# Kernel tuning notes

Hardware: AMD Instinct MI355X
Metric: run time of the kernel (lower is better)

## Reference

```python
import jax, jax.numpy as jnp
import numpy as np

D_MODEL = 1024
NUM_HEADS = 16
D_FF = 4096
MAX_SEQ_LEN = 2048
THETA = 10000.0
EPS = 1e-5
B, S = 2, 2048


def setup_inputs() -> dict:
    key = jax.random.key(0)
    ks = jax.random.split(key, 10)
    scale = 0.02
    inp = {
        "in_features": jax.random.normal(ks[0], (B, S, D_MODEL), dtype=jnp.float32),
        "token_positions": jnp.broadcast_to(jnp.arange(S, dtype=jnp.int32), (B, S)),
        "q_w": jax.random.normal(ks[1], (D_MODEL, D_MODEL), dtype=jnp.float32) * scale,
        "k_w": jax.random.normal(ks[2], (D_MODEL, D_MODEL), dtype=jnp.float32) * scale,
        "v_w": jax.random.normal(ks[3], (D_MODEL, D_MODEL), dtype=jnp.float32) * scale,
        "o_w": jax.random.normal(ks[4], (D_MODEL, D_MODEL), dtype=jnp.float32) * scale,
        "ln1_w": jnp.ones((D_MODEL,), dtype=jnp.float32),
        "ln2_w": jnp.ones((D_MODEL,), dtype=jnp.float32),
        "ffn_w1": jax.random.normal(ks[5], (D_FF, D_MODEL), dtype=jnp.float32) * scale,
        "ffn_w2": jax.random.normal(ks[6], (D_MODEL, D_FF), dtype=jnp.float32) * scale,
        "ffn_w3": jax.random.normal(ks[7], (D_FF, D_MODEL), dtype=jnp.float32) * scale,
    }
    return inp


def _rmsnorm(x, w, eps=EPS):
    return x * jax.lax.rsqrt(jnp.mean(x * x, axis=-1, keepdims=True) + eps) * w


def _rope(x, pos, theta=THETA):
    # x: [B, H, S, Dh]; pos: [B, S] int
    dh = x.shape[-1]
    inv_freq = theta ** (-jnp.arange(0, dh, 2, dtype=jnp.float32) / dh)  # [Dh/2]
    ang = pos.astype(jnp.float32)[..., None] * inv_freq                  # [B, S, Dh/2]
    cos = jnp.cos(ang)[:, None, :, :]  # [B, 1, S, Dh/2]
    sin = jnp.sin(ang)[:, None, :, :]
    x1, x2 = x[..., 0::2], x[..., 1::2]
    r1 = x1 * cos - x2 * sin
    r2 = x1 * sin + x2 * cos
    return jnp.stack([r1, r2], axis=-1).reshape(x.shape)


def _block(x, pos, q_w, k_w, v_w, o_w, ln1_w, ln2_w, w1, w2, w3):
    b, s, d = x.shape
    h, dh = NUM_HEADS, d // NUM_HEADS
    # Pre-LN attention
    xn = _rmsnorm(x, ln1_w)
    q = jnp.einsum('bsd,ed->bse', xn, q_w).reshape(b, s, h, dh).transpose(0, 2, 1, 3)
    k = jnp.einsum('bsd,ed->bse', xn, k_w).reshape(b, s, h, dh).transpose(0, 2, 1, 3)
    v = jnp.einsum('bsd,ed->bse', xn, v_w).reshape(b, s, h, dh).transpose(0, 2, 1, 3)
    q = _rope(q, pos)
    k = _rope(k, pos)
    scores = jnp.einsum('bhqd,bhkd->bhqk', q, k) / jnp.sqrt(jnp.float32(dh))
    causal = jnp.tril(jnp.ones((s, s), dtype=bool))
    scores = jnp.where(causal, scores, jnp.float32(-1e9))
    attn = jax.nn.softmax(scores, axis=-1)
    ctx = jnp.einsum('bhqk,bhkd->bhqd', attn, v).transpose(0, 2, 1, 3).reshape(b, s, d)
    attn_out = jnp.einsum('bsd,ed->bse', ctx, o_w)
    x = x + attn_out
    # Pre-LN SwiGLU FFN
    xn2 = _rmsnorm(x, ln2_w)
    g = jnp.einsum('bsd,fd->bsf', xn2, w1)
    u = jnp.einsum('bsd,fd->bsf', xn2, w3)
    ffn_out = jnp.einsum('bsf,df->bsd', jax.nn.silu(g) * u, w2)
    return x + ffn_out


def reference(in_features, token_positions, q_w, k_w, v_w, o_w, ln1_w, ln2_w, ffn_w1, ffn_w2, ffn_w3):
    return _block(in_features, token_positions, q_w, k_w, v_w, o_w, ln1_w, ln2_w, ffn_w1, ffn_w2, ffn_w3)
```

## Files before the change

kernel.cpp:

```cpp
#include <hip/hip_runtime.h>
#include <hip/hip_bf16.h>

typedef __attribute__((ext_vector_type(8))) __bf16 bf16x8;
typedef __attribute__((ext_vector_type(4))) float f32x4;
typedef __attribute__((ext_vector_type(16))) float f32x16;

#define DEV static __device__ __forceinline__

DEV unsigned short f2bf(float f) {
  __bf16 h = (__bf16)f;
  union { __bf16 h; unsigned short u; } v; v.h = h;
  return v.u;
}
DEV float bf2f(unsigned short h) {
  union { unsigned int u; float f; } v; v.u = ((unsigned int)h) << 16;
  return v.f;
}
DEV unsigned pkbf(float lo, float hi) {
  union { __bf16 h[2]; unsigned u; } v;
  v.h[0] = (__bf16)lo; v.h[1] = (__bf16)hi;
  return v.u;
}
DEV f32x4 mfma16(bf16x8 a, bf16x8 b, f32x4 c) {
  return __builtin_amdgcn_mfma_f32_16x16x32_bf16(a, b, c, 0, 0, 0);
}
DEV f32x16 mfma32(bf16x8 a, bf16x8 b, f32x16 c) {
  return __builtin_amdgcn_mfma_f32_32x32x16_bf16(a, b, c, 0, 0, 0);
}
DEV void gload_lds16(const void* g, void* l) {
  __builtin_amdgcn_global_load_lds((__attribute__((address_space(1))) void*)g,
                                   (__attribute__((address_space(3))) void*)l,
                                   16, 0, 0);
}
DEV float fexp2(float x) { return exp2f(x); }

struct CvtArgs { const float* src[7]; int cum[8]; };
__global__ __launch_bounds__(256) void cvt_all(CvtArgs a, unsigned short* __restrict__ dst) {
  int i = (blockIdx.x * 256 + threadIdx.x) * 4;
  if (i >= a.cum[7]) return;
  int w = 0;
#pragma unroll 7
  for (int t = 0; t < 7; ++t) if (i >= a.cum[t + 1]) w = t + 1;
  float4 v = *(const float4*)(a.src[w] + (i - a.cum[w]));
  dst[i + 0] = f2bf(v.x);
  dst[i + 1] = f2bf(v.y);
  dst[i + 2] = f2bf(v.z);
  dst[i + 3] = f2bf(v.w);
}

__global__ __launch_bounds__(256) void rmsnorm_k(const float* __restrict__ x,
                                                 const float* __restrict__ w,
                                                 unsigned short* __restrict__ out) {
  int row = blockIdx.x;
  int tid = threadIdx.x;
  const float* xr = x + (size_t)row * 1024;
  float4 v = *(const float4*)(xr + tid * 4);
  float ss = v.x * v.x + v.y * v.y + v.z * v.z + v.w * v.w;
#pragma unroll
  for (int m = 32; m >= 1; m >>= 1) ss += __shfl_xor(ss, m);
  __shared__ float red[4];
  int wid = tid >> 6;
  if ((tid & 63) == 0) red[wid] = ss;
  __syncthreads();
  float tot = red[0] + red[1] + red[2] + red[3];
  float rs = rsqrtf(tot * (1.0f / 1024.0f) + 1e-5f);
  float4 wv = *(const float4*)(w + tid * 4);
  unsigned short* o = out + (size_t)row * 1024 + tid * 4;
  o[0] = f2bf(v.x * rs * wv.x);
  o[1] = f2bf(v.y * rs * wv.y);
  o[2] = f2bf(v.z * rs * wv.z);
  o[3] = f2bf(v.w * rs * wv.w);
}

__global__ __launch_bounds__(256) void rope2_k(unsigned short* __restrict__ q,
                                               unsigned short* __restrict__ k,
                                               const int* __restrict__ pos) {
  int gid = blockIdx.x * 256 + threadIdx.x;
  unsigned short* x = (gid < 2097152) ? q : k;
  int idx = gid & 2097151;
  int i = idx & 31;
  int s = (idx >> 5) & 2047;
  int bh = idx >> 16;
  int b = bh >> 4;
  float p = (float)pos[b * 2048 + s];
  float inv = exp2f(-(float)i * 0.4152410118609203f);
  float ang = p * inv;
  float sn = sinf(ang), cs = cosf(ang);
  size_t base = (((size_t)bh * 2048) + s) * 64 + 2 * i;
  float x1 = bf2f(x[base]), x2 = bf2f(x[base + 1]);
  x[base]     = f2bf(x1 * cs - x2 * sn);
  x[base + 1] = f2bf(x1 * sn + x2 * cs);
}

template <int MODE>
DEV void gemm8_body(const unsigned short* __restrict__ A, int lda,
                    const unsigned short* __restrict__ B, int ldb,
                    int bm, int bn, int kbase, int nt,
                    unsigned short* __restrict__ outb, float* __restrict__ outf,
                    const float* __restrict__ resid, const unsigned short* __restrict__ gate,
                    unsigned short* As, unsigned short* Bs) {
  const int tid = threadIdx.x;
  const int lane = tid & 63, wid = tid >> 6;
  const int wr = wid >> 2, wc = wid & 3;
  const int m0 = bm * 256, n0 = bn * 256;

  const int r0 = tid >> 2, r1 = 128 + (tid >> 2), cc = tid & 3;
  const int sc0 = (cc ^ ((r0 >> 1) & 3)) * 8;
  const int sc1 = (cc ^ ((r1 >> 1) & 3)) * 8;
  const size_t arow0 = (size_t)(m0 + r0) * lda, arow1 = (size_t)(m0 + r1) * lda;
  const size_t brow0 = (size_t)(n0 + r0) * ldb, brow1 = (size_t)(n0 + r1) * ldb;
  const int du0 = tid * 8, du1 = (512 + tid) * 8;

  auto stA = [&](int t, int kh) {
    unsigned short* d = As + ((((t & 1) << 1) | kh) * 8192);
    const unsigned short* s = A + kbase + t * 64 + kh * 32;
    gload_lds16(s + arow0 + sc0, d + du0);
    gload_lds16(s + arow1 + sc1, d + du1);
  };
  auto stB = [&](int t, int kh) {
    unsigned short* d = Bs + ((((t & 1) << 1) | kh) * 8192);
    const unsigned short* s = B + kbase + t * 64 + kh * 32;
    gload_lds16(s + brow0 + sc0, d + du0);
    gload_lds16(s + brow1 + sc1, d + du1);
  };

  const int fcol = ((lane >> 4) ^ ((lane >> 1) & 3)) * 8;
  const int frow = lane & 15;
  const int abase = (wr * 128 + frow) * 32 + fcol;
  const int bbase = (wc * 64 + frow) * 32 + fcol;

  f32x4 acc[8][4] = {};
  bf16x8 a[4], b[4];

#define LOADA(buf, ks, mh) { const unsigned short* p_ = As + (((buf) << 1) | (ks)) * 8192 + abase + (mh) * 2048; \
  a[0] = *(const bf16x8*)(p_); a[1] = *(const bf16x8*)(p_ + 512); \
  a[2] = *(const bf16x8*)(p_ + 1024); a[3] = *(const bf16x8*)(p_ + 1536); }
#define LOADB(buf, ks) { const unsigned short* p_ = Bs + (((buf) << 1) | (ks)) * 8192 + bbase; \
  b[0] = *(const bf16x8*)(p_); b[1] = *(const bf16x8*)(p_ + 512); \
  b[2] = *(const bf16x8*)(p_ + 1024); b[3] = *(const bf16x8*)(p_ + 1536); }
#define MFMAQ(mh) { _Pragma("unroll") for (int fi = 0; fi < 4; ++fi) \
  _Pragma("unroll") for (int j = 0; j < 4; ++j) \
    acc[(mh) * 4 + fi][j] = mfma16(a[fi], b[j], acc[(mh) * 4 + fi][j]); }
#define LGK0() { asm volatile("s_waitcnt lgkmcnt(0)" ::: "memory"); __builtin_amdgcn_sched_barrier(0); }

  stA(0, 0); stB(0, 0); stA(0, 1); stB(0, 1);
  stA(1, 0); stB(1, 0);
  asm volatile("s_waitcnt vmcnt(4)" ::: "memory");
  __builtin_amdgcn_s_barrier();

  for (int t = 0; t < nt; ++t) {
    const int buf = t & 1;
    LOADA(buf, 0, 0); LOADB(buf, 0);
    if (t + 1 < nt) stA(t + 1, 1);
    __builtin_amdgcn_s_barrier();
    LGK0();
    __builtin_amdgcn_s_setprio(1); MFMAQ(0); __builtin_amdgcn_s_setprio(0);
    __builtin_amdgcn_s_barrier();
    LOADA(buf, 0, 1);
    if (t + 1 < nt) stB(t + 1, 1);
    __builtin_amdgcn_s_barrier();
    LGK0();
    __builtin_amdgcn_s_setprio(1); MFMAQ(1); __builtin_amdgcn_s_setprio(0);
    __builtin_amdgcn_s_barrier();
    LOADA(buf, 1, 0); LOADB(buf, 1);
    if (t + 2 < nt) stA(t + 2, 0);
    __builtin_amdgcn_s_barrier();
    LGK0();
    __builtin_amdgcn_s_setprio(1); MFMAQ(0); __builtin_amdgcn_s_setprio(0);
    __builtin_amdgcn_s_barrier();
    LOADA(buf, 1, 1);
    if (t + 2 < nt) stB(t + 2, 0);
    __builtin_amdgcn_s_barrier();
    LGK0();
    __builtin_amdgcn_s_setprio(1); MFMAQ(1); __builtin_amdgcn_s_setprio(0);
    if (t + 1 < nt) {
      if (t + 2 < nt) { asm volatile("s_waitcnt vmcnt(4)" ::: "memory"); }
      else            { asm volatile("s_waitcnt vmcnt(0)" ::: "memory"); }
      __builtin_amdgcn_s_barrier();
    }
  }
#undef LOADA
#undef LOADB
#undef MFMAQ
#undef LGK0

#pragma unroll
  for (int i = 0; i < 8; ++i)
#pragma unroll
    for (int j = 0; j < 4; ++j)
#pragma unroll
      for (int r = 0; r < 4; ++r) {
        int m = m0 + wr * 128 + i * 16 + ((lane >> 4) << 2) + r;
        int n = n0 + wc * 64 + j * 16 + (lane & 15);
        float v = acc[i][j][r];
        if (MODE == 0) {
          unsigned short* dst = outb + ((n >= 1024) ? 4194304 : 0);
          int nn = n & 1023;
          int bb = m >> 11, s = m & 2047, hh = nn >> 6, dd = nn & 63;
          dst[(((size_t)bb * 16 + hh) * 2048 + s) * 64 + dd] = f2bf(v);
        } else if (MODE == 1) {
          int hh = m >> 6, dd = m & 63, bb = n >> 11, s = n & 2047;
          outb[(((size_t)bb * 16 + hh) * 64 + dd) * 2048 + s] = f2bf(v);
        } else if (MODE == 2) {
          size_t idx = (size_t)m * 1024 + n;
          outf[idx] = resid[idx] + v;
        } else if (MODE == 3) {
          outb[(size_t)m * 4096 + n] = f2bf(v);
        } else if (MODE == 4) {
          size_t idx = (size_t)m * 4096 + n;
          float g = bf2f(gate[idx]);
          outb[idx] = f2bf(g / (1.0f + __expf(-g)) * v);
        } else {
          outf[(size_t)m * 1024 + n] = v;
        }
      }
}

DEV void swz_map(int bid, int nwg, int MT, int& bm, int& bn) {
  int cpx = nwg >> 3;
  int sw = (bid & 7) * cpx + (bid >> 3);
  bm = sw % MT;
  bn = sw / MT;
}

template <int MODE>
__global__ __launch_bounds__(512, 2) void gemm8_k(const unsigned short* __restrict__ A, int lda,
                                                  const unsigned short* __restrict__ B, int ldb,
                                                  int MT, int kz, int nt,
                                                  unsigned short* __restrict__ outb,
                                                  float* __restrict__ outf,
                                                  const float* __restrict__ resid,
                                                  const unsigned short* __restrict__ gate) {
  __shared__ __align__(16) unsigned short lds[65536];
  int bm, bn;
  swz_map(blockIdx.x, gridDim.x, MT, bm, bn);
  int kb = kz * blockIdx.y;
  float* of = outf;
  if (MODE == 5) of += (size_t)blockIdx.y * 4194304;
  gemm8_body<MODE>(A, lda, B, ldb, bm, bn, kb, nt, outb, of, resid, gate, lds, lds + 32768);
}

__global__ __launch_bounds__(512, 2) void gemm8_qkv(const unsigned short* __restrict__ xn,
                                                    const unsigned short* __restrict__ wqk,
                                                    const unsigned short* __restrict__ wv,
                                                    unsigned short* __restrict__ qk_out,
                                                    unsigned short* __restrict__ vt_out) {
  __shared__ __align__(16) unsigned short lds[65536];
  int bid = blockIdx.x;
  if (bid < 128) {
    int bm, bn;
    swz_map(bid, 128, 16, bm, bn);
    gemm8_body<0>(xn, 1024, wqk, 1024, bm, bn, 0, 16, qk_out, nullptr, nullptr, nullptr, lds, lds + 32768);
  } else {
    bid -= 128;
    int bm, bn;
    swz_map(bid, 64, 4, bm, bn);
    gemm8_body<1>(wv, 1024, xn, 1024, bm, bn, 0, 16, vt_out, nullptr, nullptr, nullptr, lds, lds + 32768);
  }
}

__global__ __launch_bounds__(256) void gemm_wo(const unsigned short* __restrict__ A,
                                               const unsigned short* __restrict__ Bw,
                                               float* __restrict__ outf,
                                               const float* __restrict__ resid) {
  __shared__ __align__(16) unsigned short As[128 * 64];
  __shared__ __align__(16) unsigned short Bs[128 * 64];
  const int K = 1024, N = 1024;
  const int tid = threadIdx.x;
  const int wid = tid >> 6, lane = tid & 63;
  const int wr = wid >> 1, wc = wid & 1;
  const int m0 = blockIdx.x * 128, n0 = blockIdx.y * 128;
  const int sw = (lane & 7) * 8;
  f32x4 acc[4][4] = {};

  for (int k0 = 0; k0 < K; k0 += 64) {
    __syncthreads();
#pragma unroll
    for (int it = 0; it < 4; ++it) {
      int c = wid * 4 + it;
      int row = c * 8 + (lane >> 3);
      int col = ((lane & 7) ^ (row & 7)) * 8;
      gload_lds16(A + (size_t)(m0 + row) * K + k0 + col, As + c * 512);
      gload_lds16(Bw + (size_t)(n0 + row) * K + k0 + col, Bs + c * 512);
    }
    asm volatile("s_waitcnt vmcnt(0)" ::: "memory");
    __syncthreads();
#pragma unroll
    for (int kk = 0; kk < 2; ++kk) {
      const int kof = (kk * 32 + (lane >> 4) * 8) ^ sw;
      bf16x8 af[4], bfr[4];
#pragma unroll
      for (int i = 0; i < 4; ++i) {
        af[i]  = *(const bf16x8*)(As + (wr * 64 + i * 16 + (lane & 15)) * 64 + kof);
        bfr[i] = *(const bf16x8*)(Bs + (wc * 64 + i * 16 + (lane & 15)) * 64 + kof);
      }
#pragma unroll
      for (int i = 0; i < 4; ++i)
#pragma unroll
        for (int j = 0; j < 4; ++j) acc[i][j] = mfma16(af[i], bfr[j], acc[i][j]);
    }
  }
  const int rb = m0 + wr * 64 + ((lane >> 4) * 4);
  const int cb = n0 + wc * 64 + (lane & 15);
#pragma unroll
  for (int i = 0; i < 4; ++i)
#pragma unroll
    for (int r = 0; r < 4; ++r) {
      int m = rb + i * 16 + r;
#pragma unroll
      for (int j = 0; j < 4; ++j) {
        size_t idx = (size_t)m * N + cb + j * 16;
        outf[idx] = resid[idx] + acc[i][j][r];
      }
    }
}

__global__ __launch_bounds__(256) void reduce_k(float* __restrict__ out,
                                                const float* __restrict__ part) {
  int i = (blockIdx.x * 256 + threadIdx.x) * 4;
  float4 o = *(const float4*)(out + i);
  float4 p0 = *(const float4*)(part + i);
  float4 p1 = *(const float4*)(part + 4194304 + i);
  float4 p2 = *(const float4*)(part + 8388608 + i);
  float4 p3 = *(const float4*)(part + 12582912 + i);
  o.x += p0.x + p1.x + p2.x + p3.x;
  o.y += p0.y + p1.y + p2.y + p3.y;
  o.z += p0.z + p1.z + p2.z + p3.z;
  o.w += p0.w + p1.w + p2.w + p3.w;
  *(float4*)(out + i) = o;
}

__global__ __launch_bounds__(256) void attn_k(const unsigned short* __restrict__ q,
                                              const unsigned short* __restrict__ k,
                                              const unsigned short* __restrict__ vt,
                                              unsigned short* __restrict__ ctx) {
  __shared__ __align__(16) unsigned short Ks[2][4096];
  __shared__ __align__(16) unsigned short Vs[2][4096];
  const int bid = blockIdx.x;
  const int bh = (bid & 7) * 4 + ((bid >> 3) & 3);
  const int qtile = 15 - (bid >> 5);
  const int tid = threadIdx.x, wid = tid >> 6, lane = tid & 63;
  const int l31 = lane & 31, hi = lane >> 5;
  const size_t bhS = (size_t)bh * 2048;
  const size_t bhD = (size_t)bh * 64 * 2048;
  const int b = bh >> 4, hh = bh & 15;
  const float SC2 = 0.18033688011112042f;

  const int c0 = wid * 2, c1 = c0 + 1;
  const int rl0 = c0 * 4 + (lane >> 4), rl1 = c1 * 4 + (lane >> 4);
  const int u0 = ((lane & 15) ^ (rl0 & 15)) * 8;
  const int u1 = ((lane & 15) ^ (rl1 & 15)) * 8;
  const int sr0 = rl0 + ((u0 >> 6) << 5), scol0 = u0 & 63;
  const int sr1 = rl1 + ((u1 >> 6) << 5), scol1 = u1 & 63;

  auto stage = [&](int kt, int buf) {
    gload_lds16(k + (bhS + kt * 64 + sr0) * 64 + scol0, &Ks[buf][c0 * 512]);
    gload_lds16(k + (bhS + kt * 64 + sr1) * 64 + scol1, &Ks[buf][c1 * 512]);
    gload_lds16(vt + bhD + (size_t)sr0 * 2048 + kt * 64 + scol0, &Vs[buf][c0 * 512]);
    gload_lds16(vt + bhD + (size_t)sr1 * 2048 + kt * 64 + scol1, &Vs[buf][c1 * 512]);
  };

  const int qrow = qtile * 128 + wid * 32 + l31;
  bf16x8 qf[4];
  {
    const unsigned short* qp = q + (bhS + qrow) * 64 + hi * 8;
#pragma unroll
    for (int c = 0; c < 4; ++c) {
      bf16x8 t = *(const bf16x8*)(qp + c * 16);
#pragma unroll
      for (int j = 0; j < 8; ++j) t[j] = (__bf16)((float)t[j] * SC2);
      qf[c] = t;
    }
  }

  float mrow = -1e30f, lrow = 0.0f;
  f32x16 o0 = {}, o1 = {};
  const int qw0 = qtile * 128 + wid * 32;
  const int ktmax = (qw0 + 31) >> 6;
  const int KT = 2 * qtile + 2;
  const int rsw = (l31 & 15) * 8;

  stage(0, 0);
  stage(1, 1);
  asm volatile("s_waitcnt vmcnt(4)" ::: "memory");
  __builtin_amdgcn_s_barrier();

  for (int kt = 0; kt < KT; ++kt) {
    const int cur = kt & 1;
    if (kt <= ktmax) {
      f32x16 sa0 = {}, sa1 = {};
#pragma unroll
      for (int c = 0; c < 4; ++c) {
        int colbase = c * 16 + hi * 8;
        bf16x8 k0 = *(const bf16x8*)(&Ks[cur][l31 * 128 + (colbase ^ rsw)]);
        bf16x8 k1 = *(const bf16x8*)(&Ks[cur][l31 * 128 + ((64 + colbase) ^ rsw)]);
        sa0 = mfma32(k0, qf[c], sa0);
        sa1 = mfma32(k1, qf[c], sa1);
      }
      float s[32];
#pragma unroll
      for (int r = 0; r < 16; ++r) { s[r] = sa0[r]; s[16 + r] = sa1[r]; }
      if (kt * 64 + 63 > qw0) {
        const int qg = qw0 + l31;
#pragma unroll
        for (int r = 0; r < 16; ++r) {
          int key0 = kt * 64 + (r & 3) + 8 * (r >> 2) + 4 * hi;
          if (key0 > qg) s[r] = -3e38f;
          if (key0 + 32 > qg) s[16 + r] = -3e38f;
        }
      }
      float pmax = s[0];
#pragma unroll
      for (int r = 1; r < 32; ++r) pmax = fmaxf(pmax, s[r]);
      pmax = fmaxf(pmax, __shfl_xor(pmax, 32));
      if (!__all(pmax <= mrow + 11.5f)) {
        float mnew = fmaxf(mrow, pmax);
        float dl = mrow - mnew;
        mrow = mnew;
        lrow *= fexp2(dl);
#pragma unroll
        for (int r = 0; r < 16; ++r) {
          int qsrc = (r & 3) + 8 * (r >> 2) + 4 * hi;
          float ar = fexp2(__shfl(dl, qsrc, 64));
          o0[r] *= ar; o1[r] *= ar;
        }
      }
      float sum = 0.0f;
#pragma unroll
      for (int r = 0; r < 32; ++r) { s[r] = fexp2(s[r] - mrow); sum += s[r]; }
      lrow += sum;
      unsigned pw[16];
#pragma unroll
      for (int i = 0; i < 16; ++i) pw[i] = pkbf(s[2 * i], s[2 * i + 1]);
#pragma unroll
      for (int g = 0; g < 4; ++g) {
        asm volatile("v_permlane32_swap_b32 %0, %1" : "+v"(pw[4 * g]), "+v"(pw[4 * g + 2]));
        asm volatile("v_permlane32_swap_b32 %0, %1" : "+v"(pw[4 * g + 1]), "+v"(pw[4 * g + 3]));
      }
#pragma unroll
      for (int g = 0; g < 4; ++g) {
        union { unsigned w[4]; bf16x8 v; } pa;
        pa.w[0] = pw[4 * g]; pa.w[1] = pw[4 * g + 1];
        pa.w[2] = pw[4 * g + 2]; pa.w[3] = pw[4 * g + 3];
        int kl = g * 16 + hi * 8;
        bf16x8 v0 = *(const bf16x8*)(&Vs[cur][l31 * 128 + (kl ^ rsw)]);
        bf16x8 v1 = *(const bf16x8*)(&Vs[cur][l31 * 128 + ((64 + kl) ^ rsw)]);
        o0 = mfma32(pa.v, v0, o0);
        o1 = mfma32(pa.v, v1, o1);
      }
    }
    __builtin_amdgcn_s_barrier();
    if (kt + 2 < KT) {
      stage(kt + 2, cur);
      asm volatile("s_waitcnt vmcnt(4)" ::: "memory");
    } else if (kt + 1 < KT) {
      asm volatile("s_waitcnt vmcnt(0)" ::: "memory");
    }
    __builtin_amdgcn_s_barrier();
  }

  lrow += __shfl_xor(lrow, 32);
  float inv = 1.0f / lrow;
#pragma unroll
  for (int r = 0; r < 16; ++r) {
    int qsrc = (r & 3) + 8 * (r >> 2) + 4 * hi;
    float li = __shfl(inv, qsrc, 64);
    int srow = qtile * 128 + wid * 32 + qsrc;
    size_t base = ((size_t)b * 2048 + srow) * 1024 + hh * 64 + l31;
    ctx[base]      = f2bf(o0[r] * li);
    ctx[base + 32] = f2bf(o1[r] * li);
  }
}

extern "C" void kernel_launch(void* const* d_in, const int* in_sizes, int n_in,
                              void* d_out, int out_size, void* d_ws, size_t ws_size,
                              hipStream_t stream) {
  (void)in_sizes; (void)n_in; (void)out_size; (void)ws_size;
  const float* in_f = (const float*)d_in[0];
  const int* pos    = (const int*)d_in[1];
  const float* q_w  = (const float*)d_in[2];
  const float* k_w  = (const float*)d_in[3];
  const float* v_w  = (const float*)d_in[4];
  const float* o_w  = (const float*)d_in[5];
  const float* ln1  = (const float*)d_in[6];
  const float* ln2  = (const float*)d_in[7];
  const float* w1   = (const float*)d_in[8];
  const float* w2   = (const float*)d_in[9];
  const float* w3   = (const float*)d_in[10];
  float* out = (float*)d_out;

  unsigned short* ws = (unsigned short*)d_ws;
  unsigned short* wb   = ws;
  unsigned short* wqkb = wb;
  unsigned short* wvb  = wb + 2097152;
  unsigned short* wob  = wb + 3145728;
  unsigned short* w1b  = wb + 4194304;
  unsigned short* w2b  = wb + 8388608;
  unsigned short* w3b  = wb + 12582912;
  unsigned short* xn   = ws + 16777216;
  unsigned short* qb   = ws + 20971520;
  unsigned short* kb   = ws + 25165824;
  unsigned short* vb   = ws + 29360128;
  unsigned short* cx   = ws + 33554432;
  unsigned short* gb   = ws + 37748736;
  float* part          = (float*)(ws + 20971520);
  unsigned short* hb   = ws + 54525952;

  CvtArgs ca;
  ca.src[0] = q_w; ca.src[1] = k_w; ca.src[2] = v_w; ca.src[3] = o_w;
  ca.src[4] = w1;  ca.src[5] = w2;  ca.src[6] = w3;
  ca.cum[0] = 0;        ca.cum[1] = 1048576;  ca.cum[2] = 2097152;  ca.cum[3] = 3145728;
  ca.cum[4] = 4194304;  ca.cum[5] = 8388608;  ca.cum[6] = 12582912; ca.cum[7] = 16777216;
  cvt_all<<<16384, 256, 0, stream>>>(ca, wb);

  rmsnorm_k<<<4096, 256, 0, stream>>>(in_f, ln1, xn);

  gemm8_qkv<<<192, 512, 0, stream>>>(xn, wqkb, wvb, qb, vb);

  rope2_k<<<16384, 256, 0, stream>>>(qb, kb, pos);

  attn_k<<<512, 256, 0, stream>>>(qb, kb, vb, cx);

  gemm_wo<<<dim3(32, 8), 256, 0, stream>>>(cx, wob, out, in_f);

  rmsnorm_k<<<4096, 256, 0, stream>>>(out, ln2, xn);

  gemm8_k<3><<<256, 512, 0, stream>>>(xn, 1024, w1b, 1024, 16, 0, 16, gb, nullptr, nullptr, nullptr);
  gemm8_k<4><<<256, 512, 0, stream>>>(xn, 1024, w3b, 1024, 16, 0, 16, hb, nullptr, nullptr, gb);
  gemm8_k<5><<<dim3(64, 4), 512, 0, stream>>>(hb, 4096, w2b, 4096, 16, 1024, 16, nullptr, part, nullptr, nullptr);

  reduce_k<<<4096, 256, 0, stream>>>(out, part);
}
```

Before: 302.0 us.

## Split attention KV range across two wave groups with in-block softmax merge

Doubles the attention block to 512 threads. The two 4-wave groups each process half of the causal key tiles for the same 128 query rows, with their own double-buffered LDS staging. At the end, group 1 writes its partial output (as bf16) and its running max and sum to LDS, and group 0 merges them flash-decoding style before writing ctx. The aim is to halve the serial key-loop length per block and raise parallelism on long-causal tiles. In exchange it uses more LDS and registers per block, adds a merge step, and rounds the partial output to bf16 before merging.

Measured after the change: 314.0 us. 4.0% more time.

```diff
diff --git a/kernel.cpp b/kernel.cpp
--- a/kernel.cpp
+++ b/kernel.cpp
@@ -330,37 +330,45 @@
   *(float4*)(out + i) = o;
 }
 
-__global__ __launch_bounds__(256) void attn_k(const unsigned short* __restrict__ q,
-                                              const unsigned short* __restrict__ k,
-                                              const unsigned short* __restrict__ vt,
-                                              unsigned short* __restrict__ ctx) {
-  __shared__ __align__(16) unsigned short Ks[2][4096];
-  __shared__ __align__(16) unsigned short Vs[2][4096];
+__global__ __launch_bounds__(512, 4) void attn_k(const unsigned short* __restrict__ q,
+                                                 const unsigned short* __restrict__ k,
+                                                 const unsigned short* __restrict__ vt,
+                                                 unsigned short* __restrict__ ctx) {
+  __shared__ __align__(16) unsigned short Ks[16384];
+  __shared__ __align__(16) unsigned short Vs[16384];
   const int bid = blockIdx.x;
-  const int bh = (bid & 7) * 4 + ((bid >> 3) & 3);
-  const int qtile = 15 - (bid >> 5);
+  const int xcd = bid & 7, inner = bid >> 3;
+  const int bh = xcd * 4 + (inner & 3);
+  const int qtile = 15 - (inner >> 2);
   const int tid = threadIdx.x, wid = tid >> 6, lane = tid & 63;
+  const int w4 = wid & 3, g = wid >> 2;
   const int l31 = lane & 31, hi = lane >> 5;
   const size_t bhS = (size_t)bh * 2048;
   const size_t bhD = (size_t)bh * 64 * 2048;
   const int b = bh >> 4, hh = bh & 15;
   const float SC2 = 0.18033688011112042f;
 
-  const int c0 = wid * 2, c1 = c0 + 1;
+  const int NT = qtile + 1;
+  const int kb = g * NT;
+
+  const int c0 = w4 * 2, c1 = c0 + 1;
   const int rl0 = c0 * 4 + (lane >> 4), rl1 = c1 * 4 + (lane >> 4);
   const int u0 = ((lane & 15) ^ (rl0 & 15)) * 8;
   const int u1 = ((lane & 15) ^ (rl1 & 15)) * 8;
   const int sr0 = rl0 + ((u0 >> 6) << 5), scol0 = u0 & 63;
   const int sr1 = rl1 + ((u1 >> 6) << 5), scol1 = u1 & 63;
-
-  auto stage = [&](int kt, int buf) {
-    gload_lds16(k + (bhS + kt * 64 + sr0) * 64 + scol0, &Ks[buf][c0 * 512]);
-    gload_lds16(k + (bhS + kt * 64 + sr1) * 64 + scol1, &Ks[buf][c1 * 512]);
-    gload_lds16(vt + bhD + (size_t)sr0 * 2048 + kt * 64 + scol0, &Vs[buf][c0 * 512]);
-    gload_lds16(vt + bhD + (size_t)sr1 * 2048 + kt * 64 + scol1, &Vs[buf][c1 * 512]);
+  unsigned short* KsG = Ks + g * 8192;
+  unsigned short* VsG = Vs + g * 8192;
+
+  auto stage = [&](int ktl, int buf) {
+    int kt = kb + ktl;
+    gload_lds16(k + (bhS + kt * 64 + sr0) * 64 + scol0, KsG + buf * 4096 + c0 * 512);
+    gload_lds16(k + (bhS + kt * 64 + sr1) * 64 + scol1, KsG + buf * 4096 + c1 * 512);
+    gload_lds16(vt + bhD + (size_t)sr0 * 2048 + kt * 64 + scol0, VsG + buf * 4096 + c0 * 512);
+    gload_lds16(vt + bhD + (size_t)sr1 * 2048 + kt * 64 + scol1, VsG + buf * 4096 + c1 * 512);
   };
 
-  const int qrow = qtile * 128 + wid * 32 + l31;
+  const int qrow = qtile * 128 + w4 * 32 + l31;
   bf16x8 qf[4];
   {
     const unsigned short* qp = q + (bhS + qrow) * 64 + hi * 8;
@@ -375,9 +383,7 @@
 
   float mrow = -1e30f, lrow = 0.0f;
   f32x16 o0 = {}, o1 = {};
-  const int qw0 = qtile * 128 + wid * 32;
-  const int ktmax = (qw0 + 31) >> 6;
-  const int KT = 2 * qtile + 2;
+  const int qw0 = qtile * 128 + w4 * 32;
   const int rsw = (l31 & 15) * 8;
 
   stage(0, 0);
@@ -385,90 +391,134 @@
   asm volatile("s_waitcnt vmcnt(4)" ::: "memory");
   __builtin_amdgcn_s_barrier();
 
-  for (int kt = 0; kt < KT; ++kt) {
-    const int cur = kt & 1;
-    if (kt <= ktmax) {
-      f32x16 sa0 = {}, sa1 = {};
-#pragma unroll
-      for (int c = 0; c < 4; ++c) {
-        int colbase = c * 16 + hi * 8;
-        bf16x8 k0 = *(const bf16x8*)(&Ks[cur][l31 * 128 + (colbase ^ rsw)]);
-        bf16x8 k1 = *(const bf16x8*)(&Ks[cur][l31 * 128 + ((64 + colbase) ^ rsw)]);
-        sa0 = mfma32(k0, qf[c], sa0);
-        sa1 = mfma32(k1, qf[c], sa1);
+  for (int ktl = 0; ktl < NT; ++ktl) {
+    const int cur = ktl & 1;
+    const int kt = kb + ktl;
+    f32x16 sa0 = {}, sa1 = {};
+#pragma unroll
+    for (int c = 0; c < 4; ++c) {
+      int colbase = c * 16 + hi * 8;
+      bf16x8 k0 = *(const bf16x8*)(&KsG[cur * 4096 + l31 * 128 + (colbase ^ rsw)]);
+      bf16x8 k1 = *(const bf16x8*)(&KsG[cur * 4096 + l31 * 128 + ((64 + colbase) ^ rsw)]);
+      sa0 = mfma32(k0, qf[c], sa0);
+      sa1 = mfma32(k1, qf[c], sa1);
+    }
+    float s[32];
+#pragma unroll
+    for (int r = 0; r < 16; ++r) { s[r] = sa0[r]; s[16 + r] = sa1[r]; }
+    if (kt * 64 + 63 > qw0) {
+      const int qg = qw0 + l31;
+#pragma unroll
+      for (int r = 0; r < 16; ++r) {
+        int key0 = kt * 64 + (r & 3) + 8 * (r >> 2) + 4 * hi;
+        if (key0 > qg) s[r] = -3e38f;
+        if (key0 + 32 > qg) s[16 + r] = -3e38f;
       }
-      float s[32];
-#pragma unroll
-      for (int r = 0; r < 16; ++r) { s[r] = sa0[r]; s[16 + r] = sa1[r]; }
-      if (kt * 64 + 63 > qw0) {
-        const int qg = qw0 + l31;
-#pragma unroll
-        for (int r = 0; r < 16; ++r) {
-          int key0 = kt * 64 + (r & 3) + 8 * (r >> 2) + 4 * hi;
-          if (key0 > qg) s[r] = -3e38f;
-          if (key0 + 32 > qg) s[16 + r] = -3e38f;
-        }
+    }
+    float pmax = s[0];
+#pragma unroll
+    for (int r = 1; r < 32; ++r) pmax = fmaxf(pmax, s[r]);
+    pmax = fmaxf(pmax, __shfl_xor(pmax, 32));
+    if (!__all(pmax <= mrow + 11.5f)) {
+      float mnew = fmaxf(mrow, pmax);
+      float dl = mrow - mnew;
+      mrow = mnew;
+      lrow *= fexp2(dl);
+#pragma unroll
+      for (int r = 0; r < 16; ++r) {
+        int qsrc = (r & 3) + 8 * (r >> 2) + 4 * hi;
+        float ar = fexp2(__shfl(dl, qsrc, 64));
+        o0[r] *= ar; o1[r] *= ar;
       }
-      float pmax = s[0];
-#pragma unroll
-      for (int r = 1; r < 32; ++r) pmax = fmaxf(pmax, s[r]);
-      pmax = fmaxf(pmax, __shfl_xor(pmax, 32));
-      if (!__all(pmax <= mrow + 11.5f)) {
-        float mnew = fmaxf(mrow, pmax);
-        float dl = mrow - mnew;
-        mrow = mnew;
-        lrow *= fexp2(dl);
-#pragma unroll
-        for (int r = 0; r < 16; ++r) {
-          int qsrc = (r & 3) + 8 * (r >> 2) + 4 * hi;
-          float ar = fexp2(__shfl(dl, qsrc, 64));
-          o0[r] *= ar; o1[r] *= ar;
-        }
-      }
-      float sum = 0.0f;
-#pragma unroll
-      for (int r = 0; r < 32; ++r) { s[r] = fexp2(s[r] - mrow); sum += s[r]; }
-      lrow += sum;
-      unsigned pw[16];
-#pragma unroll
-      for (int i = 0; i < 16; ++i) pw[i] = pkbf(s[2 * i], s[2 * i + 1]);
-#pragma unroll
-      for (int g = 0; g < 4; ++g) {
-        asm volatile("v_permlane32_swap_b32 %0, %1" : "+v"(pw[4 * g]), "+v"(pw[4 * g + 2]));
-        asm volatile("v_permlane32_swap_b32 %0, %1" : "+v"(pw[4 * g + 1]), "+v"(pw[4 * g + 3]));
-      }
-#pragma unroll
-      for (int g = 0; g < 4; ++g) {
-        union { unsigned w[4]; bf16x8 v; } pa;
-        pa.w[0] = pw[4 * g]; pa.w[1] = pw[4 * g + 1];
-        pa.w[2] = pw[4 * g + 2]; pa.w[3] = pw[4 * g + 3];
-        int kl = g * 16 + hi * 8;
-        bf16x8 v0 = *(const bf16x8*)(&Vs[cur][l31 * 128 + (kl ^ rsw)]);
-        bf16x8 v1 = *(const bf16x8*)(&Vs[cur][l31 * 128 + ((64 + kl) ^ rsw)]);
-        o0 = mfma32(pa.v, v0, o0);
-        o1 = mfma32(pa.v, v1, o1);
-      }
-    }
-    __builtin_amdgcn_s_barrier();
-    if (kt + 2 < KT) {
-      stage(kt + 2, cur);
+    }
+    float sum = 0.0f;
+#pragma unroll
+    for (int r = 0; r < 32; ++r) { s[r] = fexp2(s[r] - mrow); sum += s[r]; }
+    lrow += sum;
+    unsigned pw[16];
+#pragma unroll
+    for (int i = 0; i < 16; ++i) pw[i] = pkbf(s[2 * i], s[2 * i + 1]);
+#pragma unroll
+    for (int gg = 0; gg < 4; ++gg) {
+      asm volatile("v_permlane32_swap_b32 %0, %1" : "+v"(pw[4 * gg]), "+v"(pw[4 * gg + 2]));
+      asm volatile("v_permlane32_swap_b32 %0, %1" : "+v"(pw[4 * gg + 1]), "+v"(pw[4 * gg + 3]));
+    }
+#pragma unroll
+    for (int gg = 0; gg < 4; ++gg) {
+      union { unsigned w[4]; bf16x8 v; } pa;
+      pa.w[0] = pw[4 * gg]; pa.w[1] = pw[4 * gg + 1];
+      pa.w[2] = pw[4 * gg + 2]; pa.w[3] = pw[4 * gg + 3];
+      int kl = gg * 16 + hi * 8;
+      bf16x8 v0 = *(const bf16x8*)(&VsG[cur * 4096 + l31 * 128 + (kl ^ rsw)]);
+      bf16x8 v1 = *(const bf16x8*)(&VsG[cur * 4096 + l31 * 128 + ((64 + kl) ^ rsw)]);
+      o0 = mfma32(pa.v, v0, o0);
+      o1 = mfma32(pa.v, v1, o1);
+    }
+    __builtin_amdgcn_s_barrier();
+    if (ktl + 2 < NT) {
+      stage(ktl + 2, cur);
       asm volatile("s_waitcnt vmcnt(4)" ::: "memory");
-    } else if (kt + 1 < KT) {
+    } else if (ktl + 1 < NT) {
       asm volatile("s_waitcnt vmcnt(0)" ::: "memory");
     }
     __builtin_amdgcn_s_barrier();
   }
 
   lrow += __shfl_xor(lrow, 32);
-  float inv = 1.0f / lrow;
-#pragma unroll
-  for (int r = 0; r < 16; ++r) {
-    int qsrc = (r & 3) + 8 * (r >> 2) + 4 * hi;
-    float li = __shfl(inv, qsrc, 64);
-    int srow = qtile * 128 + wid * 32 + qsrc;
-    size_t base = ((size_t)b * 2048 + srow) * 1024 + hh * 64 + l31;
-    ctx[base]      = f2bf(o0[r] * li);
-    ctx[base + 32] = f2bf(o1[r] * li);
+
+  asm volatile("s_waitcnt vmcnt(0)" ::: "memory");
+  __builtin_amdgcn_s_barrier();
+
+  unsigned* Obw = (unsigned*)Ks;
+  float* mlp = (float*)Vs;
+
+  if (g == 1) {
+    int ob = (w4 * 64 + lane) * 16;
+    unsigned tmp[16];
+#pragma unroll
+    for (int i = 0; i < 8; ++i) tmp[i] = pkbf(o0[2 * i], o0[2 * i + 1]);
+#pragma unroll
+    for (int i = 0; i < 8; ++i) tmp[8 + i] = pkbf(o1[2 * i], o1[2 * i + 1]);
+#pragma unroll
+    for (int c = 0; c < 4; ++c)
+      *(uint4*)(&Obw[ob + 4 * c]) = make_uint4(tmp[4 * c], tmp[4 * c + 1], tmp[4 * c + 2], tmp[4 * c + 3]);
+    if (hi == 0) {
+      mlp[(w4 * 32 + l31) * 2]     = mrow;
+      mlp[(w4 * 32 + l31) * 2 + 1] = lrow;
+    }
+  }
+  __builtin_amdgcn_s_barrier();
+
+  if (g == 0) {
+    float m1 = mlp[(w4 * 32 + l31) * 2];
+    float l1 = mlp[(w4 * 32 + l31) * 2 + 1];
+    float mF = fmaxf(mrow, m1);
+    float a0 = fexp2(mrow - mF);
+    float a1 = fexp2(m1 - mF);
+    float lF = lrow * a0 + l1 * a1;
+    float inv = 1.0f / lF;
+    int ob = (w4 * 64 + lane) * 16;
+    unsigned od[16];
+#pragma unroll
+    for (int c = 0; c < 4; ++c) {
+      uint4 t = *(const uint4*)(&Obw[ob + 4 * c]);
+      od[4 * c] = t.x; od[4 * c + 1] = t.y; od[4 * c + 2] = t.z; od[4 * c + 3] = t.w;
+    }
+#pragma unroll
+    for (int r = 0; r < 16; ++r) {
+      int qsrc = (r & 3) + 8 * (r >> 2) + 4 * hi;
+      float a0r = __shfl(a0, qsrc, 64);
+      float a1r = __shfl(a1, qsrc, 64);
+      float invr = __shfl(inv, qsrc, 64);
+      float ob0 = bf2f((unsigned short)((od[r >> 1] >> ((r & 1) * 16)) & 0xffff));
+      float ob1 = bf2f((unsigned short)((od[8 + (r >> 1)] >> ((r & 1) * 16)) & 0xffff));
+      float v0 = (o0[r] * a0r + ob0 * a1r) * invr;
+      float v1 = (o1[r] * a0r + ob1 * a1r) * invr;
+      int srow = qtile * 128 + w4 * 32 + qsrc;
+      size_t base = ((size_t)b * 2048 + srow) * 1024 + hh * 64 + l31;
+      ctx[base]      = f2bf(v0);
+      ctx[base + 32] = f2bf(v1);
+    }
   }
 }
 
@@ -519,7 +569,7 @@
 
   rope2_k<<<16384, 256, 0, stream>>>(qb, kb, pos);
 
-  attn_k<<<512, 256, 0, stream>>>(qb, kb, vb, cx);
+  attn_k<<<512, 512, 0, stream>>>(qb, kb, vb, cx);
 
   gemm_wo<<<dim3(32, 8), 256, 0, stream>>>(cx, wob, out, in_f);
 
```
